# Kernel tuning notes

Hardware: AMD Instinct MI355X
Metric: run time of the kernel (lower is better)

Reference implementation:

```python
import jax, jax.numpy as jnp
import numpy as np
from jax import lax

D_MODEL, D_INNER, D_STATE, D_CONV, DT_RANK = 1024, 2048, 16, 4, 64
B_SZ, L = 2, 2048


def silu(v):
    return v * jax.nn.sigmoid(v)


def setup_inputs() -> dict:
    key = jax.random.key(0)
    ks = jax.random.split(key, 9)
    s = 0.02
    x = jax.random.normal(ks[0], (B_SZ, L, D_MODEL), jnp.float32)
    W_in = jax.random.normal(ks[1], (D_MODEL, 2 * D_INNER), jnp.float32) * s
    conv_w = jax.random.normal(ks[2], (D_INNER, D_CONV), jnp.float32) * 0.1  # depthwise kernel
    conv_b = jax.random.normal(ks[3], (D_INNER,), jnp.float32) * 0.01
    W_xproj = jax.random.normal(ks[4], (D_INNER, DT_RANK + 2 * D_STATE), jnp.float32) * s
    W_dt = jax.random.normal(ks[5], (DT_RANK, D_INNER), jnp.float32) * s
    b_dt = jax.random.normal(ks[6], (D_INNER,), jnp.float32) * 0.01
    A_log = jnp.log(jnp.tile(jnp.arange(1, D_STATE + 1, dtype=jnp.float32), (D_INNER, 1)))
    D = jnp.ones((D_INNER,), jnp.float32)
    W_out = jax.random.normal(ks[7], (D_INNER, D_MODEL), jnp.float32) * s
    return dict(x=x, W_in=W_in, conv_w=conv_w, conv_b=conv_b, W_xproj=W_xproj,
                W_dt=W_dt, b_dt=b_dt, A_log=A_log, D=D, W_out=W_out)


def reference(x, W_in, conv_w, conv_b, W_xproj, W_dt, b_dt, A_log, D, W_out):
    # in_proj, split into conv path u and gate res
    xr = x @ W_in                                  # (B, L, 2*d_inner)
    u, res = jnp.split(xr, 2, axis=-1)
    # causal depthwise conv1d (left-pad d_conv-1), then SiLU
    uc = jnp.swapaxes(u, 1, 2)                     # (B, C, L)
    uc = lax.conv_general_dilated(
        uc, conv_w[:, None, :], window_strides=(1,),
        padding=[(D_CONV - 1, 0)], feature_group_count=D_INNER,
        dimension_numbers=('NCH', 'OIH', 'NCH'))
    uc = uc + conv_b[None, :, None]
    u = silu(jnp.swapaxes(uc, 1, 2))               # (B, L, d_inner)
    # S6 projections
    x_dbl = u @ W_xproj                            # (B, L, dt_rank + 2*N)
    dt_low = x_dbl[..., :DT_RANK]
    Bm = x_dbl[..., DT_RANK:DT_RANK + D_STATE]     # (B, L, N)
    Cm = x_dbl[..., DT_RANK + D_STATE:]            # (B, L, N)
    dt = jax.nn.softplus(dt_low @ W_dt + b_dt)     # (B, L, d_inner)
    A = -jnp.exp(A_log)                            # (d_inner, N)
    # selective scan over time
    def step(h, inp):
        dt_t, B_t, C_t, u_t = inp                  # (B,d), (B,N), (B,N), (B,d)
        dA = jnp.exp(dt_t[:, :, None] * A)         # (B, d, N)
        dBu = dt_t[:, :, None] * B_t[:, None, :] * u_t[:, :, None]
        h = dA * h + dBu
        y = jnp.sum(h * C_t[:, None, :], axis=-1)  # (B, d)
        return h, y
    h0 = jnp.zeros((B_SZ, D_INNER, D_STATE), u.dtype)
    xs = (jnp.swapaxes(dt, 0, 1), jnp.swapaxes(Bm, 0, 1),
          jnp.swapaxes(Cm, 0, 1), jnp.swapaxes(u, 0, 1))
    _, ys = lax.scan(step, h0, xs)
    y = jnp.swapaxes(ys, 0, 1) + u * D             # (B, L, d_inner)
    # gate and out_proj
    y = y * silu(res)
    return y @ W_out
```

## Files before the change

kernel.cpp:

```cpp
#include <hip/hip_runtime.h>
#include <cstdint>
#include <cstddef>

#define DMODEL 1024
#define DINNER 2048
#define DSTATE 16
#define DCONV  4
#define DTRANK 64
#define BSZ    2
#define SEQL   2048
#define MROWS  (BSZ*SEQL)
#define NCHUNK 32
#define CLEN   (SEQL/NCHUNK)

typedef __bf16 bf16;
typedef bf16  bf16x8 __attribute__((ext_vector_type(8)));
typedef bf16  bf16x4 __attribute__((ext_vector_type(4)));
typedef float floatx4 __attribute__((ext_vector_type(4)));

#define EPILDC 136

__device__ __forceinline__ float fsigmoid(float x){ return 1.f/(1.f+__expf(-x)); }
__device__ __forceinline__ float fsilu(float x){ return x*fsigmoid(x); }

__device__ __forceinline__ void gload_lds16(const void* g, void* l){
  __builtin_amdgcn_global_load_lds((__attribute__((address_space(1))) void*)g,
                                   (__attribute__((address_space(3))) void*)l,
                                   16, 0, 0);
}

__global__ void k_cast_bf16(const float* __restrict__ in, bf16* __restrict__ out, int n){
  int i = (blockIdx.x*blockDim.x + threadIdx.x)*4;
  if (i < n){
    float4 v = *(const float4*)(in + i);
    bf16x4 o; o[0]=(bf16)v.x; o[1]=(bf16)v.y; o[2]=(bf16)v.z; o[3]=(bf16)v.w;
    *(bf16x4*)(out + i) = o;
  }
}

__global__ void k_transpose_all(const float* __restrict__ W_in, const float* __restrict__ W_out,
                                const float* __restrict__ W_xproj, const float* __restrict__ W_dt,
                                bf16* __restrict__ WinT, bf16* __restrict__ WoutT,
                                bf16* __restrict__ WxT, bf16* __restrict__ WdtT){
  __shared__ float tile[32][33];
  int b = blockIdx.x;
  const float* in; bf16* out; int R, C, outR, nbx;
  if      (b < 4096)            { in=W_in;    out=WinT;  R=1024; C=4096; outR=4096; nbx=128; }
  else if (b < 4096+2048)       { b-=4096;    in=W_out;  out=WoutT; R=2048; C=1024; outR=1024; nbx=32; }
  else if (b < 4096+2048+256)   { b-=6144;    in=W_xproj;out=WxT;  R=2048; C=96;   outR=128;  nbx=4; }
  else                          { b-=6400;    in=W_dt;   out=WdtT; R=64;   C=2048; outR=2048; nbx=64; }
  int c0 = (b % nbx)*32, r0 = (b / nbx)*32;
  int tx = threadIdx.x, ty = threadIdx.y;
  #pragma unroll
  for (int ii=0; ii<4; ++ii){
    int r = r0 + ty + ii*8, c = c0 + tx;
    float v = 0.f;
    if (r < R && c < C) v = in[(size_t)r*C + c];
    tile[ty+ii*8][tx] = v;
  }
  __syncthreads();
  #pragma unroll
  for (int ii=0; ii<4; ++ii){
    int orow = c0 + ty + ii*8;
    int ocol = r0 + tx;
    if (orow < outR && ocol < R) out[(size_t)orow*R + ocol] = (bf16)tile[tx][ty+ii*8];
  }
}

template<int EPI>
__global__ __launch_bounds__(256)
void k_gemm_bt(const bf16* __restrict__ A, const bf16* __restrict__ Bt,
               int M, int N, int K,
               float* __restrict__ C0, bf16* __restrict__ C1, bf16* __restrict__ C2,
               const float* __restrict__ bias){
  __shared__ bf16 lds[128*EPILDC];
  bf16* ldsA = lds;
  bf16* ldsB = lds + 8192;
  const int tid  = threadIdx.x;
  const int lane = tid & 63;
  const int wave = tid >> 6;
  const int quad = lane >> 4;
  const int mrow = lane & 15;
  const int wr = wave >> 1, wc = wave & 1;
  const int bm = blockIdx.y * 128, bn = blockIdx.x * 128;
  const int Ks   = K / gridDim.z;
  const int kbeg = blockIdx.z * Ks;

  floatx4 acc[4][4];
  #pragma unroll
  for (int i=0;i<4;++i)
    #pragma unroll
    for (int j=0;j<4;++j) acc[i][j] = (floatx4){0.f,0.f,0.f,0.f};

  const int r_local = tid >> 3;
  const int cs = (((tid & 7) ^ (r_local & 7)) * 8);
  const bf16* Abase = A  + (size_t)(bm + r_local) * K + cs;
  const bf16* Bbase = Bt + (size_t)(bn + r_local) * K + cs;
  const int swz = mrow & 7;

  for (int k0 = kbeg; k0 < kbeg + Ks; k0 += 64){
    #pragma unroll
    for (int p=0;p<4;++p){
      gload_lds16(Abase + k0 + (size_t)p*32*K, ldsA + (p*256 + tid)*8);
      gload_lds16(Bbase + k0 + (size_t)p*32*K, ldsB + (p*256 + tid)*8);
    }
    __syncthreads();

    #pragma unroll
    for (int kk=0; kk<2; ++kk){
      const int qs = quad + kk*4;
      bf16x8 af[4], bfr[4];
      #pragma unroll
      for (int i=0;i<4;++i)
        af[i] = *(const bf16x8*)(ldsA + (wr*64 + i*16 + mrow)*64 + ((qs ^ swz))*8);
      #pragma unroll
      for (int j=0;j<4;++j)
        bfr[j] = *(const bf16x8*)(ldsB + (wc*64 + j*16 + mrow)*64 + ((qs ^ swz))*8);
      #pragma unroll
      for (int i=0;i<4;++i)
        #pragma unroll
        for (int j=0;j<4;++j)
          acc[i][j] = __builtin_amdgcn_mfma_f32_16x16x32_bf16(af[i], bfr[j], acc[i][j], 0,0,0);
    }
    __syncthreads();
  }

  if (EPI == 0){
    float* Cz = C0 + (size_t)blockIdx.z * M * N;
    #pragma unroll
    for (int i=0;i<4;++i){
      #pragma unroll
      for (int r=0;r<4;++r){
        int row = bm + wr*64 + i*16 + quad*4 + r;
        #pragma unroll
        for (int j=0;j<4;++j){
          int col = bn + wc*64 + j*16 + mrow;
          Cz[(size_t)row*N + col] = acc[i][j][r];
        }
      }
    }
  } else {
    const bool isres = (EPI == 1) && (bn >= DINNER);
    #pragma unroll
    for (int i=0;i<4;++i){
      #pragma unroll
      for (int r=0;r<4;++r){
        int lrow = wr*64 + i*16 + quad*4 + r;
        #pragma unroll
        for (int j=0;j<4;++j){
          int lcol = wc*64 + j*16 + mrow;
          float v = acc[i][j][r];
          float vt;
          if (EPI == 1) vt = isres ? fsilu(v) : v;
          else {
            float z = v + bias[bn + lcol];
            vt = (z > 20.f) ? z : log1pf(__expf(z));
          }
          lds[lrow*EPILDC + lcol] = (bf16)vt;
        }
      }
    }
    __syncthreads();
    bf16* dst; int ldc;
    if (EPI == 1){ ldc = DINNER; dst = isres ? (C2 + (bn - DINNER)) : (C1 + bn); }
    else         { ldc = N;      dst = C1 + bn; }
    const int rr = tid >> 1, hh = (tid & 1)*64;
    #pragma unroll
    for (int i=0;i<8;++i)
      *(bf16x8*)(dst + (size_t)(bm + rr)*ldc + hh + i*8) =
        *(const bf16x8*)(lds + rr*EPILDC + hh + i*8);
  }
}

__global__ void k_xdbl_reduce(const float* __restrict__ part, float* __restrict__ xdbl,
                              bf16* __restrict__ dtlowb){
  int t = blockIdx.x*blockDim.x + threadIdx.x;
  int i4 = t*4;
  floatx4 acc = (floatx4){0.f,0.f,0.f,0.f};
  #pragma unroll
  for (int z=0; z<8; ++z)
    acc += *(const floatx4*)(part + (size_t)z*MROWS*128 + i4);
  *(floatx4*)(xdbl + i4) = acc;
  int r = i4 >> 7, c = i4 & 127;
  if (c < DTRANK){
    bf16x4 o; o[0]=(bf16)acc[0]; o[1]=(bf16)acc[1]; o[2]=(bf16)acc[2]; o[3]=(bf16)acc[3];
    *(bf16x4*)(dtlowb + (size_t)r*DTRANK + c) = o;
  }
}

__global__ void k_out_reduce(const float* __restrict__ part, float* __restrict__ out){
  int i4 = (blockIdx.x*blockDim.x + threadIdx.x)*4;
  floatx4 a = *(const floatx4*)(part + i4);
  floatx4 b = *(const floatx4*)(part + (size_t)MROWS*DMODEL + i4);
  *(floatx4*)(out + i4) = a + b;
}

__global__ void k_conv_silu(const bf16* __restrict__ u_pre,
                            const float* __restrict__ conv_w,
                            const float* __restrict__ conv_b,
                            bf16* __restrict__ ub){
  int t   = blockIdx.x*blockDim.x + threadIdx.x;
  int d4  = (t & (DINNER/4-1))*4;
  int row = t >> 9;
  int l   = row & (SEQL-1);
  float4 cb = *(const float4*)(conv_b + d4);
  float acc[4] = {cb.x, cb.y, cb.z, cb.w};
  float4 w0 = *(const float4*)(conv_w + (d4+0)*4);
  float4 w1 = *(const float4*)(conv_w + (d4+1)*4);
  float4 w2 = *(const float4*)(conv_w + (d4+2)*4);
  float4 w3 = *(const float4*)(conv_w + (d4+3)*4);
  float wk[4][4] = {{w0.x,w0.y,w0.z,w0.w},{w1.x,w1.y,w1.z,w1.w},
                    {w2.x,w2.y,w2.z,w2.w},{w3.x,w3.y,w3.z,w3.w}};
  #pragma unroll
  for (int k=0;k<4;++k){
    int lk = l + k - 3;
    if (lk >= 0){
      bf16x4 uv = *(const bf16x4*)(u_pre + (size_t)(row + k - 3)*DINNER + d4);
      #pragma unroll
      for (int j=0;j<4;++j) acc[j] += (float)uv[j] * wk[j][k];
    }
  }
  bf16x4 o;
  #pragma unroll
  for (int j=0;j<4;++j) o[j] = (bf16)fsilu(acc[j]);
  *(bf16x4*)(ub + (size_t)row*DINNER + d4) = o;
}

__global__ void k_scan_phase1(const bf16* __restrict__ dt, const bf16* __restrict__ ub,
                              const float* __restrict__ x_dbl, const float* __restrict__ A_log,
                              float* __restrict__ Pbuf, float* __restrict__ Sbuf){
  int t  = blockIdx.x*blockDim.x + threadIdx.x;
  int g  = t & 3;
  int d  = (t >> 2) & (DINNER-1);
  int bc = t >> 13;
  int c  = bc & (NCHUNK-1);
  int b  = bc >> 5;
  floatx4 alog = *(const floatx4*)(A_log + d*DSTATE + g*4);
  float an[4];
  #pragma unroll
  for (int n=0;n<4;++n) an[n] = -__expf(alog[n]);
  float P[4] = {1.f,1.f,1.f,1.f}, S[4] = {0.f,0.f,0.f,0.f};
  int base_row = b*SEQL + c*CLEN;
  for (int s=0;s<CLEN;++s){
    size_t row = base_row + s;
    float dtv = (float)dt[row*DINNER + d];
    float uv  = (float)ub[row*DINNER + d];
    float du  = dtv*uv;
    floatx4 Bv = *(const floatx4*)(x_dbl + row*128 + DTRANK + g*4);
    #pragma unroll
    for (int n=0;n<4;++n){
      float e = __expf(dtv*an[n]);
      P[n] *= e;
      S[n]  = fmaf(S[n], e, du*Bv[n]);
    }
  }
  size_t ob = ((size_t)bc*DINNER + d)*DSTATE + g*4;
  floatx4 Pv = {P[0],P[1],P[2],P[3]}, Sv = {S[0],S[1],S[2],S[3]};
  *(floatx4*)(Pbuf + ob) = Pv;
  *(floatx4*)(Sbuf + ob) = Sv;
}

__global__ void k_scan_phase2(const float* __restrict__ Pbuf, float* __restrict__ Sbuf){
  int t = blockIdx.x*blockDim.x + threadIdx.x;
  int b   = t >> 15;
  int rem = t & 32767;
  float h = 0.f;
  for (int c=0;c<NCHUNK;++c){
    size_t ix = (size_t)(b*NCHUNK + c)*DINNER*DSTATE + rem;
    float p = Pbuf[ix], s = Sbuf[ix];
    Sbuf[ix] = h;
    h = fmaf(p, h, s);
  }
}

__global__ void k_scan_phase3(const bf16* __restrict__ dt, const bf16* __restrict__ ub,
                              const float* __restrict__ x_dbl, const float* __restrict__ A_log,
                              const float* __restrict__ Dvec, const float* __restrict__ Hin,
                              const bf16* __restrict__ resb, bf16* __restrict__ yb){
  int t  = blockIdx.x*blockDim.x + threadIdx.x;
  int g  = t & 3;
  int d  = (t >> 2) & (DINNER-1);
  int bc = t >> 13;
  int c  = bc & (NCHUNK-1);
  int b  = bc >> 5;
  floatx4 alog = *(const floatx4*)(A_log + d*DSTATE + g*4);
  float an[4];
  #pragma unroll
  for (int n=0;n<4;++n) an[n] = -__expf(alog[n]);
  floatx4 h = *(const floatx4*)(Hin + ((size_t)bc*DINNER + d)*DSTATE + g*4);
  float Dd = Dvec[d];
  int base_row = b*SEQL + c*CLEN;
  for (int s=0;s<CLEN;++s){
    size_t row = base_row + s;
    float dtv = (float)dt[row*DINNER + d];
    float uv  = (float)ub[row*DINNER + d];
    float du  = dtv*uv;
    floatx4 Bv = *(const floatx4*)(x_dbl + row*128 + DTRANK + g*4);
    floatx4 Cv = *(const floatx4*)(x_dbl + row*128 + DTRANK + DSTATE + g*4);
    float y = 0.f;
    #pragma unroll
    for (int n=0;n<4;++n){
      float e = __expf(dtv*an[n]);
      h[n] = fmaf(h[n], e, du*Bv[n]);
      y = fmaf(h[n], Cv[n], y);
    }
    y += __shfl_xor(y, 1);
    y += __shfl_xor(y, 2);
    if (g == 0){
      y = (y + uv*Dd) * (float)resb[row*DINNER + d];
      yb[row*DINNER + d] = (bf16)y;
    }
  }
}

extern "C" void kernel_launch(void* const* d_in, const int* in_sizes, int n_in,
                              void* d_out, int out_size, void* d_ws, size_t ws_size,
                              hipStream_t stream){
  const float* x      = (const float*)d_in[0];
  const float* W_in   = (const float*)d_in[1];
  const float* conv_w = (const float*)d_in[2];
  const float* conv_b = (const float*)d_in[3];
  const float* W_xproj= (const float*)d_in[4];
  const float* W_dt   = (const float*)d_in[5];
  const float* b_dt   = (const float*)d_in[6];
  const float* A_log  = (const float*)d_in[7];
  const float* Dv     = (const float*)d_in[8];
  const float* W_out  = (const float*)d_in[9];
  float* out = (float*)d_out;

  uint8_t* wp = (uint8_t*)d_ws;
  auto alloc = [&](size_t bytes)->void*{ void* p = wp; wp += (bytes + 255) & ~(size_t)255; return p; };
  bf16*  xb     = (bf16*) alloc((size_t)MROWS*DMODEL*2);
  bf16*  WinT   = (bf16*) alloc((size_t)2*DINNER*DMODEL*2);
  bf16*  WoutT  = (bf16*) alloc((size_t)DMODEL*DINNER*2);
  bf16*  WxT    = (bf16*) alloc((size_t)128*DINNER*2);
  bf16*  WdtT   = (bf16*) alloc((size_t)DINNER*DTRANK*2);
  bf16*  updt   = (bf16*) alloc((size_t)MROWS*DINNER*2);
  float* scanPS = (float*)alloc((size_t)2*BSZ*NCHUNK*DSTATE*DINNER*4);
  float* Pbuf   = scanPS;
  float* Sbuf   = scanPS + (size_t)BSZ*NCHUNK*DSTATE*DINNER;
  float* xdbl_part = scanPS;
  float* outpart   = (float*)updt;
  bf16*  resb   = (bf16*) alloc((size_t)MROWS*DINNER*2);
  bf16*  ub     = (bf16*) alloc((size_t)MROWS*DINNER*2);
  float* xdbl   = (float*)alloc((size_t)MROWS*128*4);
  bf16*  dtlowb = (bf16*) alloc((size_t)MROWS*DTRANK*2);
  bf16*  yb     = (bf16*) alloc((size_t)MROWS*DINNER*2);

  k_cast_bf16<<<(MROWS*DMODEL/4 + 255)/256, 256, 0, stream>>>(x, xb, MROWS*DMODEL);
  k_transpose_all<<<4096+2048+256+128, dim3(32,8), 0, stream>>>(W_in, W_out, W_xproj, W_dt,
                                                                WinT, WoutT, WxT, WdtT);

  k_gemm_bt<1><<<dim3(4096/128, 4096/128), 256, 0, stream>>>(xb, WinT, MROWS, 2*DINNER, DMODEL, nullptr, updt, resb, nullptr);
  k_conv_silu<<<MROWS*DINNER/4/256, 256, 0, stream>>>(updt, conv_w, conv_b, ub);
  k_gemm_bt<0><<<dim3(1, 4096/128, 8), 256, 0, stream>>>(ub, WxT, MROWS, 128, DINNER, xdbl_part, nullptr, nullptr, nullptr);
  k_xdbl_reduce<<<(MROWS*128/4)/256, 256, 0, stream>>>(xdbl_part, xdbl, dtlowb);
  k_gemm_bt<2><<<dim3(2048/128, 4096/128), 256, 0, stream>>>(dtlowb, WdtT, MROWS, DINNER, DTRANK, nullptr, updt, nullptr, b_dt);
  k_scan_phase1<<<BSZ*NCHUNK*DINNER*4/256, 256, 0, stream>>>(updt, ub, xdbl, A_log, Pbuf, Sbuf);
  k_scan_phase2<<<BSZ*DINNER*DSTATE/256, 256, 0, stream>>>(Pbuf, Sbuf);
  k_scan_phase3<<<BSZ*NCHUNK*DINNER*4/256, 256, 0, stream>>>(updt, ub, xdbl, A_log, Dv, Sbuf, resb, yb);
  k_gemm_bt<0><<<dim3(1024/128, 4096/128, 2), 256, 0, stream>>>(yb, WoutT, MROWS, DMODEL, DINNER, outpart, nullptr, nullptr, nullptr);
  k_out_reduce<<<(MROWS*DMODEL/4)/256, 256, 0, stream>>>(outpart, out);
}
```

Before: 368.4 us.

## Double-buffer GEMM LDS tiles with K-step 32 to overlap loads and MFMA

Restructures the bf16 GEMM main loop to use two LDS buffers with a 32-wide K slice each. The next slice is prefetched into the alternate buffer while MFMAs run on the current one, leaving one barrier per iteration. The swizzle is adapted to the narrower rows, and a barrier is added before the epilogue reuses LDS. This aims to hide global-load latency, at the cost of twice as many loop iterations with less MFMA work per barrier.

```diff
diff --git a/kernel.cpp b/kernel.cpp
--- a/kernel.cpp
+++ b/kernel.cpp
@@ -73,9 +73,7 @@
                int M, int N, int K,
                float* __restrict__ C0, bf16* __restrict__ C1, bf16* __restrict__ C2,
                const float* __restrict__ bias){
-  __shared__ bf16 lds[128*EPILDC];
-  bf16* ldsA = lds;
-  bf16* ldsB = lds + 8192;
+  __shared__ bf16 lds[17408];
   const int tid  = threadIdx.x;
   const int lane = tid & 63;
   const int wave = tid >> 6;
@@ -92,37 +90,43 @@
     #pragma unroll
     for (int j=0;j<4;++j) acc[i][j] = (floatx4){0.f,0.f,0.f,0.f};
 
-  const int r_local = tid >> 3;
-  const int cs = (((tid & 7) ^ (r_local & 7)) * 8);
-  const bf16* Abase = A  + (size_t)(bm + r_local) * K + cs;
-  const bf16* Bbase = Bt + (size_t)(bn + r_local) * K + cs;
-  const int swz = mrow & 7;
-
-  for (int k0 = kbeg; k0 < kbeg + Ks; k0 += 64){
-    #pragma unroll
-    for (int p=0;p<4;++p){
-      gload_lds16(Abase + k0 + (size_t)p*32*K, ldsA + (p*256 + tid)*8);
-      gload_lds16(Bbase + k0 + (size_t)p*32*K, ldsB + (p*256 + tid)*8);
-    }
+  const int ar0 = tid >> 2;
+  const int kc  = ((tid & 3) ^ ((ar0 >> 1) & 3)) * 8;
+  const bf16* Ag0 = A  + (size_t)(bm + ar0)      * K + kc;
+  const bf16* Ag1 = A  + (size_t)(bm + ar0 + 64) * K + kc;
+  const bf16* Bg0 = Bt + (size_t)(bn + ar0)      * K + kc;
+  const bf16* Bg1 = Bt + (size_t)(bn + ar0 + 64) * K + kc;
+  const int ksl = (mrow >> 1) & 3;
+
+  auto stage = [&](int k0, int p){
+    bf16* bA = lds + p*4096;
+    bf16* bB = lds + 8192 + p*4096;
+    gload_lds16(Ag0 + k0, bA + (size_t)tid*8);
+    gload_lds16(Ag1 + k0, bA + (size_t)(256+tid)*8);
+    gload_lds16(Bg0 + k0, bB + (size_t)tid*8);
+    gload_lds16(Bg1 + k0, bB + (size_t)(256+tid)*8);
+  };
+
+  stage(kbeg, 0);
+  int p = 0;
+  for (int k0 = kbeg; k0 < kbeg + Ks; k0 += 32){
     __syncthreads();
-
-    #pragma unroll
-    for (int kk=0; kk<2; ++kk){
-      const int qs = quad + kk*4;
-      bf16x8 af[4], bfr[4];
-      #pragma unroll
-      for (int i=0;i<4;++i)
-        af[i] = *(const bf16x8*)(ldsA + (wr*64 + i*16 + mrow)*64 + ((qs ^ swz))*8);
+    if (k0 + 32 < kbeg + Ks) stage(k0 + 32, p ^ 1);
+    const bf16* bA = lds + p*4096;
+    const bf16* bB = lds + 8192 + p*4096;
+    bf16x8 af[4], bfr[4];
+    #pragma unroll
+    for (int i=0;i<4;++i)
+      af[i] = *(const bf16x8*)(bA + (wr*64 + i*16 + mrow)*32 + (quad ^ ksl)*8);
+    #pragma unroll
+    for (int j=0;j<4;++j)
+      bfr[j] = *(const bf16x8*)(bB + (wc*64 + j*16 + mrow)*32 + (quad ^ ksl)*8);
+    #pragma unroll
+    for (int i=0;i<4;++i)
       #pragma unroll
       for (int j=0;j<4;++j)
-        bfr[j] = *(const bf16x8*)(ldsB + (wc*64 + j*16 + mrow)*64 + ((qs ^ swz))*8);
-      #pragma unroll
-      for (int i=0;i<4;++i)
-        #pragma unroll
-        for (int j=0;j<4;++j)
-          acc[i][j] = __builtin_amdgcn_mfma_f32_16x16x32_bf16(af[i], bfr[j], acc[i][j], 0,0,0);
-    }
-    __syncthreads();
+        acc[i][j] = __builtin_amdgcn_mfma_f32_16x16x32_bf16(af[i], bfr[j], acc[i][j], 0,0,0);
+    p ^= 1;
   }
 
   if (EPI == 0){
@@ -140,9 +144,10 @@
       }
     }
   } else {
+    __syncthreads();
     const bool isres = (EPI == 1) && (bn >= DINNER);
     #pragma unroll
-    for (int i=0;i<4;++i){
+    for (int i=0;i<4;++i)
       #pragma unroll
       for (int r=0;r<4;++r){
         int lrow = wr*64 + i*16 + quad*4 + r;
@@ -159,7 +164,6 @@
           lds[lrow*EPILDC + lcol] = (bf16)vt;
         }
       }
-    }
     __syncthreads();
     bf16* dst; int ldc;
     if (EPI == 1){ ldc = DINNER; dst = isres ? (C2 + (bn - DINNER)) : (C1 + bn); }
```

Result: no change. 364.3 us (-1.1%).
